# Optimization experiments

Hardware: AMD Instinct MI355X
Metric: run time of the kernel (lower is better)

Reference implementation:

```python
import jax, jax.numpy as jnp
import numpy as np

B, P, T = 128, 196, 20
VOCAB, ENC, EMB, DEC, ATTN = 10000, 2048, 512, 512, 512


def _linear_params(key, out_dim, in_dim):
    kw, kb = jax.random.split(key)
    s = 1.0 / np.sqrt(in_dim)
    W = jax.random.uniform(kw, (out_dim, in_dim), minval=-s, maxval=s, dtype=jnp.float32)
    b = jax.random.uniform(kb, (out_dim,), minval=-s, maxval=s, dtype=jnp.float32)
    return W, b


def setup_inputs() -> dict:
    key = jax.random.key(0)
    ks = jax.random.split(key, 12)
    enc_w, enc_b = _linear_params(ks[0], ATTN, ENC)
    dec_w, dec_b = _linear_params(ks[1], ATTN, DEC)
    full_w, full_b = _linear_params(ks[2], 1, ATTN)
    W_ih, b_ih = _linear_params(ks[3], 4 * DEC, EMB + ENC)
    W_hh, b_hh = _linear_params(ks[4], 4 * DEC, DEC)
    ih_w, ih_b = _linear_params(ks[5], DEC, ENC)
    ic_w, ic_b = _linear_params(ks[6], DEC, ENC)
    fc_w, fc_b = _linear_params(ks[7], VOCAB, DEC)
    return {
        "encoder_out": jax.random.normal(ks[8], (B, P, ENC), dtype=jnp.float32),
        "captions": jax.random.randint(ks[9], (B, T), 0, VOCAB, dtype=jnp.int32),
        "lengths": jax.random.randint(ks[10], (B,), 1, T + 1, dtype=jnp.int32),
        "embedding": jax.random.normal(ks[11], (VOCAB, EMB), dtype=jnp.float32),
        "enc_attn_w": enc_w, "enc_attn_b": enc_b,
        "dec_attn_w": dec_w, "dec_attn_b": dec_b,
        "full_attn_w": full_w, "full_attn_b": full_b,
        "W_ih": W_ih, "b_ih": b_ih, "W_hh": W_hh, "b_hh": b_hh,
        "init_h_w": ih_w, "init_h_b": ih_b,
        "init_c_w": ic_w, "init_c_b": ic_b,
        "fc_w": fc_w, "fc_b": fc_b,
    }


def reference(encoder_out, captions, lengths, embedding,
              enc_attn_w, enc_attn_b, dec_attn_w, dec_attn_b,
              full_attn_w, full_attn_b, W_ih, b_ih, W_hh, b_hh,
              init_h_w, init_h_b, init_c_w, init_c_b, fc_w, fc_b):
    # init hidden state from mean-pooled encoder features
    mean_enc = encoder_out.mean(axis=1)                      # [B, ENC]
    h = mean_enc @ init_h_w.T + init_h_b                      # [B, DEC]
    c = mean_enc @ init_c_w.T + init_c_b

    # loop-invariant encoder projection for additive attention
    attn_enc = jnp.einsum('bpe,ae->bpa', encoder_out, enc_attn_w) + enc_attn_b  # [B, P, ATTN]

    embs = embedding[captions]                                # [B, T, EMB]
    embs_t = jnp.swapaxes(embs, 0, 1)                         # [T, B, EMB]

    dec = h.shape[1]

    def step(carry, emb_t):
        h, c = carry
        # additive attention
        attn_dec = h @ dec_attn_w.T + dec_attn_b              # [B, ATTN]
        energy = jnp.einsum('bpa,a->bp', jax.nn.relu(attn_enc + attn_dec[:, None, :]), full_attn_w[0]) + full_attn_b[0]
        alpha = jax.nn.softmax(energy, axis=1)                # [B, P]
        context = jnp.einsum('bpe,bp->be', encoder_out, alpha)  # [B, ENC]
        # LSTMCell
        x = jnp.concatenate([emb_t, context], axis=1)
        gates = x @ W_ih.T + b_ih + h @ W_hh.T + b_hh          # [B, 4*DEC]
        i, f, g, o = jnp.split(gates, 4, axis=1)
        c_new = jax.nn.sigmoid(f) * c + jax.nn.sigmoid(i) * jnp.tanh(g)
        h_new = jax.nn.sigmoid(o) * jnp.tanh(c_new)
        preds = h_new @ fc_w.T + fc_b                          # [B, VOCAB] (dropout in eval mode = identity)
        return (h_new, c_new), (preds, alpha)

    (_, _), (outputs_t, alphas_t) = jax.lax.scan(step, (h, c), embs_t)
    outputs = jnp.swapaxes(outputs_t, 0, 1)                   # [B, T, VOCAB]
    alphas = jnp.swapaxes(alphas_t, 0, 1)                     # [B, T, P]
    return outputs, alphas
```

## Files before the change

kernel.cpp:

```cpp
#include <hip/hip_runtime.h>

constexpr int kB = 128, kP = 196, kT = 20;
constexpr int kVocab = 10000, kEnc = 2048, kEmb = 512, kDec = 512, kAttn = 512;

typedef __bf16 b16x8 __attribute__((ext_vector_type(8)));
typedef __bf16 b16x4 __attribute__((ext_vector_type(4)));
typedef float f32x4 __attribute__((ext_vector_type(4)));
typedef unsigned short u16x4 __attribute__((ext_vector_type(4)));

__device__ __forceinline__ unsigned short f2bf(float f) {
  unsigned int u = __float_as_uint(f);
  u += 0x7fffu + ((u >> 16) & 1u);
  return (unsigned short)(u >> 16);
}
__device__ __forceinline__ float bf2f(unsigned short h) {
  return __uint_as_float(((unsigned int)h) << 16);
}

__device__ __forceinline__ void async16(const void* g, void* l) {
  __builtin_amdgcn_global_load_lds(
      (const __attribute__((address_space(1))) unsigned int*)g,
      (__attribute__((address_space(3))) unsigned int*)l, 16, 0, 0);
}

__global__ __launch_bounds__(256) void gemm_ae(
    const unsigned short* __restrict__ A, const unsigned short* __restrict__ W,
    const float* __restrict__ bias, unsigned short* __restrict__ Cb, int M, int K) {
  __shared__ unsigned short sA[128 * 32];
  const int tid = threadIdx.x;
  const int lane = tid & 63, wave = tid >> 6;
  const int m0 = blockIdx.y * 128;
  const int n0 = blockIdx.x * 64;
  const int q = lane >> 4, l = lane & 15;
  const int ch0 = tid >> 7, row0 = tid & 127;
  f32x4 acc[2][4] = {};

  for (int k0 = 0; k0 < K; k0 += 32) {
    async16(A + (long)(m0 + row0) * K + k0 + ch0 * 8, &sA[(ch0 * 128 + row0) * 8]);
    async16(A + (long)(m0 + row0) * K + k0 + (ch0 + 2) * 8, &sA[((ch0 + 2) * 128 + row0) * 8]);
    b16x8 bf4[4];
#pragma unroll
    for (int j = 0; j < 4; j++)
      bf4[j] = *(const b16x8*)(W + (long)(n0 + 16 * j + l) * K + k0 + q * 8);
    __syncthreads();
    b16x8 af[2];
#pragma unroll
    for (int i = 0; i < 2; i++)
      af[i] = *(const b16x8*)&sA[(q * 128 + wave * 32 + 16 * i + l) * 8];
#pragma unroll
    for (int i = 0; i < 2; i++)
#pragma unroll
      for (int j = 0; j < 4; j++)
        acc[i][j] = __builtin_amdgcn_mfma_f32_16x16x32_bf16(af[i], bf4[j], acc[i][j], 0, 0, 0);
    __syncthreads();
  }

#pragma unroll
  for (int i = 0; i < 2; i++)
#pragma unroll
    for (int j = 0; j < 4; j++) {
      const int col = n0 + 16 * j + l;
      const float bv = bias[col];
#pragma unroll
      for (int r = 0; r < 4; r++) {
        const int row = m0 + wave * 32 + 16 * i + q * 4 + r;
        Cb[(long)row * 512 + col] = f2bf(acc[i][j][r] + bv);
      }
    }
}

template <bool A_BF16, bool OUT_BF16>
__global__ __launch_bounds__(256) void gemm_bt(
    const void* __restrict__ A_, const unsigned short* __restrict__ W,
    const float* __restrict__ bias, float* __restrict__ C,
    unsigned short* __restrict__ Cb, int M, int N, int K, long ldc) {
  const int lane = threadIdx.x & 63;
  const int wave = threadIdx.x >> 6;
  const int wm = wave >> 1, wn = wave & 1;
  const int m0 = blockIdx.y * 64 + wm * 32;
  const int n0 = blockIdx.x * 64 + wn * 32;
  const int q = lane >> 4;
  const int l = lane & 15;
  f32x4 acc[2][2] = {};
  const unsigned short* Ab = (const unsigned short*)A_;
  const float* Af = (const float*)A_;

  for (int k0 = 0; k0 < K; k0 += 32) {
    const int ka = k0 + q * 8;
    b16x8 af[2], wf[2];
#pragma unroll
    for (int i = 0; i < 2; i++) {
      int r = m0 + 16 * i + l;
      if (r >= M) r = M - 1;
      if (A_BF16) {
        af[i] = *(const b16x8*)(Ab + (long)r * K + ka);
      } else {
        const float* p = Af + (long)r * K + ka;
        const f32x4 lo = *(const f32x4*)p;
        const f32x4 hi = *(const f32x4*)(p + 4);
        b16x8 t;
#pragma unroll
        for (int j = 0; j < 4; j++) {
          ((unsigned short*)&t)[j] = f2bf(lo[j]);
          ((unsigned short*)&t)[4 + j] = f2bf(hi[j]);
        }
        af[i] = t;
      }
    }
#pragma unroll
    for (int j = 0; j < 2; j++) {
      int r = n0 + 16 * j + l;
      if (r >= N) r = N - 1;
      wf[j] = *(const b16x8*)(W + (long)r * K + ka);
    }
#pragma unroll
    for (int i = 0; i < 2; i++)
#pragma unroll
      for (int j = 0; j < 2; j++)
        acc[i][j] = __builtin_amdgcn_mfma_f32_16x16x32_bf16(af[i], wf[j], acc[i][j], 0, 0, 0);
  }

#pragma unroll
  for (int i = 0; i < 2; i++)
#pragma unroll
    for (int j = 0; j < 2; j++) {
      const int col = n0 + 16 * j + l;
      if (col >= N) continue;
      const float bv = bias ? bias[col] : 0.0f;
#pragma unroll
      for (int r = 0; r < 4; r++) {
        const int row = m0 + 16 * i + q * 4 + r;
        if (row >= M) continue;
        const float v = acc[i][j][r] + bv;
        if (OUT_BF16) Cb[(long)row * ldc + col] = f2bf(v);
        else          C[(long)row * ldc + col] = v;
      }
    }
}

__global__ __launch_bounds__(256) void adfc_kernel(
    const unsigned short* __restrict__ h_bf,
    const unsigned short* __restrict__ daw, const float* __restrict__ dab,
    float* __restrict__ ad_out,
    const unsigned short* __restrict__ fcw, const float* __restrict__ fcb,
    float* __restrict__ preds, long pred_ld) {
  const int blk = blockIdx.x;
  const unsigned short* W;
  const float* bias;
  float* out;
  long ldc;
  int N, m0, n0;
  if (blk < 16) {
    if (!ad_out) return;
    W = daw; bias = dab; out = ad_out; ldc = 512; N = 512;
    n0 = (blk & 7) * 64; m0 = (blk >> 3) * 64;
  } else {
    if (!preds) return;
    const int idx = blk - 16;
    W = fcw; bias = fcb; out = preds; ldc = pred_ld; N = kVocab;
    n0 = (idx % 157) * 64; m0 = (idx / 157) * 64;
  }
  const int lane = threadIdx.x & 63, wave = threadIdx.x >> 6;
  const int wm = wave >> 1, wn = wave & 1;
  const int q = lane >> 4, l = lane & 15;
  const int mi = m0 + wm * 32, ni = n0 + wn * 32;
  f32x4 acc[2][2] = {};

  for (int k0 = 0; k0 < 512; k0 += 64) {
    b16x8 af[2][2], wf[2][2];
#pragma unroll
    for (int u = 0; u < 2; u++) {
      const int ka = k0 + u * 32 + q * 8;
#pragma unroll
      for (int i = 0; i < 2; i++)
        af[u][i] = *(const b16x8*)(h_bf + (long)(mi + 16 * i + l) * 512 + ka);
#pragma unroll
      for (int j = 0; j < 2; j++) {
        int r = ni + 16 * j + l;
        if (r >= N) r = N - 1;
        wf[u][j] = *(const b16x8*)(W + (long)r * 512 + ka);
      }
    }
#pragma unroll
    for (int u = 0; u < 2; u++)
#pragma unroll
      for (int i = 0; i < 2; i++)
#pragma unroll
        for (int j = 0; j < 2; j++)
          acc[i][j] = __builtin_amdgcn_mfma_f32_16x16x32_bf16(af[u][i], wf[u][j], acc[i][j], 0, 0, 0);
  }
#pragma unroll
  for (int i = 0; i < 2; i++)
#pragma unroll
    for (int j = 0; j < 2; j++) {
      const int col = ni + 16 * j + l;
      if (col >= N) continue;
      const float bv = bias[col];
#pragma unroll
      for (int r = 0; r < 4; r++) {
        const int row = mi + 16 * i + q * 4 + r;
        out[(long)row * ldc + col] = acc[i][j][r] + bv;
      }
    }
}

template <bool SRC_BF16>
__global__ __launch_bounds__(256) void attn2(
    const void* __restrict__ enc_, const unsigned short* __restrict__ attn_enc_bf,
    const float* __restrict__ ad_g, const float* __restrict__ faw,
    const float* __restrict__ fab, float* __restrict__ alphas,
    unsigned short* __restrict__ ctx, int t) {
  const int b = blockIdx.x;
  const int half = blockIdx.y;
  const int tid = threadIdx.x;
  const int lane = tid & 63, wave = tid >> 6;
  __shared__ float ad_s[512];
  __shared__ float e_sm[kP];
  __shared__ float red[4];
  __shared__ float cred[128][8];

  ad_s[tid] = ad_g[b * kAttn + tid];
  ad_s[tid + 256] = ad_g[b * kAttn + tid + 256];
  __syncthreads();

  float ad8[8], w8[8];
  const int a0 = lane * 8;
#pragma unroll
  for (int j = 0; j < 8; j++) { ad8[j] = ad_s[a0 + j]; w8[j] = faw[a0 + j]; }
  const float fb0 = fab[0];
  for (int p = wave; p < kP; p += 4) {
    const b16x8 rv = *(const b16x8*)(attn_enc_bf + ((long)(b * kP + p)) * kAttn + a0);
    float s = 0.f;
#pragma unroll
    for (int j = 0; j < 8; j++)
      s += w8[j] * fmaxf(bf2f(((const unsigned short*)&rv)[j]) + ad8[j], 0.f);
#pragma unroll
    for (int off = 32; off > 0; off >>= 1) s += __shfl_down(s, off, 64);
    if (lane == 0) e_sm[p] = s + fb0;
  }
  __syncthreads();

  const float v = (tid < kP) ? e_sm[tid] : -3.0e38f;
  float m = v;
#pragma unroll
  for (int off = 32; off > 0; off >>= 1) m = fmaxf(m, __shfl_down(m, off, 64));
  if (lane == 0) red[wave] = m;
  __syncthreads();
  m = fmaxf(fmaxf(red[0], red[1]), fmaxf(red[2], red[3]));
  const float ex = (tid < kP) ? expf(v - m) : 0.f;
  float s = ex;
#pragma unroll
  for (int off = 32; off > 0; off >>= 1) s += __shfl_down(s, off, 64);
  if (lane == 0) red[wave] = s;
  __syncthreads();
  s = red[0] + red[1] + red[2] + red[3];
  __syncthreads();
  const float alpha = ex / s;
  if (tid < kP) {
    e_sm[tid] = alpha;
    if (half == 0) alphas[((long)b * kT + t) * kP + tid] = alpha;
  }
  __syncthreads();

  const int pg = tid >> 7, th = tid & 127;
  const int e = half * 1024 + th * 8;
  float a8[8] = {};
  if (SRC_BF16) {
    const unsigned short* base = (const unsigned short*)enc_ + (long)b * kP * kEnc + e;
    const int pbeg = pg * 98;
#pragma unroll 2
    for (int p = pbeg; p < pbeg + 98; p++) {
      const float a = e_sm[p];
      const b16x8 rv = *(const b16x8*)(base + (long)p * kEnc);
#pragma unroll
      for (int j = 0; j < 8; j++) a8[j] += a * bf2f(((const unsigned short*)&rv)[j]);
    }
  } else {
    const float* base = (const float*)enc_ + (long)b * kP * kEnc + e;
    const int pbeg = pg * 98;
#pragma unroll 2
    for (int p = pbeg; p < pbeg + 98; p++) {
      const float a = e_sm[p];
      const f32x4 lo = *(const f32x4*)(base + (long)p * kEnc);
      const f32x4 hi = *(const f32x4*)(base + (long)p * kEnc + 4);
#pragma unroll
      for (int j = 0; j < 4; j++) { a8[j] += a * lo[j]; a8[4 + j] += a * hi[j]; }
    }
  }
  if (pg == 1) {
#pragma unroll
    for (int j = 0; j < 8; j++) cred[th][j] = a8[j];
  }
  __syncthreads();
  if (pg == 0) {
    u16x4 o0, o1;
#pragma unroll
    for (int j = 0; j < 4; j++) {
      o0[j] = f2bf(a8[j] + cred[th][j]);
      o1[j] = f2bf(a8[4 + j] + cred[th][4 + j]);
    }
    *(u16x4*)(ctx + (long)b * kEnc + e) = o0;
    *(u16x4*)(ctx + (long)b * kEnc + e + 4) = o1;
  }
}

__global__ __launch_bounds__(256) void gemm_gates(
    const unsigned short* __restrict__ embs_t, const unsigned short* __restrict__ ctx,
    const unsigned short* __restrict__ hbf, const unsigned short* __restrict__ Wih,
    const unsigned short* __restrict__ Whh, float* __restrict__ gates_part) {
  const int lane = threadIdx.x & 63;
  const int wave = threadIdx.x >> 6;
  const int wm = wave >> 1, wn = wave & 1;
  const int m0 = blockIdx.y * 64 + wm * 32;
  const int n0 = blockIdx.x * 64 + wn * 32;
  const int z = blockIdx.z;
  const int q = lane >> 4;
  const int l = lane & 15;
  f32x4 acc[2][2] = {};
  float* gout = gates_part + (long)z * kB * 2048;

  const int kbeg = z * 768, kend = kbeg + 768;
  for (int k0 = kbeg; k0 < kend; k0 += 32) {
    b16x8 af[2], wf[2];
#pragma unroll
    for (int i = 0; i < 2; i++) {
      const int r = m0 + 16 * i + l;
      const unsigned short* p;
      if (k0 < 512)        p = embs_t + (long)r * kEmb + k0;
      else if (k0 < 2560)  p = ctx + (long)r * kEnc + (k0 - 512);
      else                 p = hbf + (long)r * kDec + (k0 - 2560);
      af[i] = *(const b16x8*)(p + q * 8);
    }
#pragma unroll
    for (int j = 0; j < 2; j++) {
      const int r = n0 + 16 * j + l;
      const unsigned short* p;
      if (k0 < 2560) p = Wih + (long)r * 2560 + k0;
      else           p = Whh + (long)r * 512 + (k0 - 2560);
      wf[j] = *(const b16x8*)(p + q * 8);
    }
#pragma unroll
    for (int i = 0; i < 2; i++)
#pragma unroll
      for (int j = 0; j < 2; j++)
        acc[i][j] = __builtin_amdgcn_mfma_f32_16x16x32_bf16(af[i], wf[j], acc[i][j], 0, 0, 0);
  }
#pragma unroll
  for (int i = 0; i < 2; i++)
#pragma unroll
    for (int j = 0; j < 2; j++) {
      const int col = n0 + 16 * j + l;
#pragma unroll
      for (int r = 0; r < 4; r++) {
        const int row = m0 + 16 * i + q * 4 + r;
        gout[(long)row * 2048 + col] = acc[i][j][r];
      }
    }
}

__global__ __launch_bounds__(256) void lstm_pw(
    const float* __restrict__ gp, const float* __restrict__ bsum,
    float* __restrict__ c, float* __restrict__ h, unsigned short* __restrict__ hbf) {
  const int idx = blockIdx.x * 256 + threadIdx.x;
  const int b = idx >> 9, d = idx & 511;
  float g4[4];
#pragma unroll
  for (int g = 0; g < 4; g++) {
    const int col = g * 512 + d;
    float s = bsum[col];
#pragma unroll
    for (int z = 0; z < 4; z++) s += gp[(long)z * kB * 2048 + (long)b * 2048 + col];
    g4[g] = s;
  }
  const float si = 1.f / (1.f + expf(-g4[0]));
  const float sf = 1.f / (1.f + expf(-g4[1]));
  const float so = 1.f / (1.f + expf(-g4[3]));
  const float cn = sf * c[idx] + si * tanhf(g4[2]);
  const float hn = so * tanhf(cn);
  c[idx] = cn;
  h[idx] = hn;
  hbf[idx] = f2bf(hn);
}

template <bool SRC_BF16>
__global__ __launch_bounds__(256) void mean_kernel(
    const void* __restrict__ enc_, unsigned short* __restrict__ mean_bf) {
  const int b = blockIdx.x;
  const int e = threadIdx.x * 8;
  float acc[8] = {};
  if (SRC_BF16) {
    const unsigned short* base = (const unsigned short*)enc_ + (long)b * kP * kEnc + e;
    for (int p = 0; p < kP; p++) {
      const b16x8 v = *(const b16x8*)(base + (long)p * kEnc);
#pragma unroll
      for (int j = 0; j < 8; j++) acc[j] += bf2f(((const unsigned short*)&v)[j]);
    }
  } else {
    const float* base = (const float*)enc_ + (long)b * kP * kEnc + e;
    for (int p = 0; p < kP; p++) {
      const f32x4 lo = *(const f32x4*)(base + (long)p * kEnc);
      const f32x4 hi = *(const f32x4*)(base + (long)p * kEnc + 4);
#pragma unroll
      for (int j = 0; j < 4; j++) { acc[j] += lo[j]; acc[4 + j] += hi[j]; }
    }
  }
#pragma unroll
  for (int j = 0; j < 8; j++)
    mean_bf[(long)b * kEnc + e + j] = f2bf(acc[j] * (1.0f / 196.0f));
}

__global__ __launch_bounds__(256) void f32_to_bf16_vec(
    const float* __restrict__ src, unsigned short* __restrict__ dst, long n4) {
  for (long i = blockIdx.x * (long)blockDim.x + threadIdx.x; i < n4;
       i += (long)gridDim.x * blockDim.x) {
    const f32x4 v = *(const f32x4*)(src + i * 4);
    u16x4 o;
#pragma unroll
    for (int j = 0; j < 4; j++) o[j] = f2bf(v[j]);
    *(u16x4*)(dst + i * 4) = o;
  }
}

__global__ __launch_bounds__(256) void gather_emb(
    const float* __restrict__ embedding, const int* __restrict__ captions,
    unsigned short* __restrict__ embs) {
  const int r = blockIdx.x;
  const int t = r >> 7, b = r & 127;
  const int cap = captions[b * kT + t];
  const float* src = embedding + (long)cap * kEmb;
  unsigned short* dst = embs + (long)r * kEmb;
  for (int i = threadIdx.x; i < kEmb; i += 256) dst[i] = f2bf(src[i]);
}

__global__ void bias_sum_k(const float* __restrict__ b1, const float* __restrict__ b2,
                           float* __restrict__ o) {
  const int i = blockIdx.x * 256 + threadIdx.x;
  if (i < 2048) o[i] = b1[i] + b2[i];
}

extern "C" void kernel_launch(void* const* d_in, const int* in_sizes, int n_in,
                              void* d_out, int out_size, void* d_ws, size_t ws_size,
                              hipStream_t stream) {
  const float* enc = (const float*)d_in[0];
  const int* captions = (const int*)d_in[1];
  const float* embedding = (const float*)d_in[3];
  const float* eaw = (const float*)d_in[4];
  const float* eab = (const float*)d_in[5];
  const float* daw = (const float*)d_in[6];
  const float* dab = (const float*)d_in[7];
  const float* faw = (const float*)d_in[8];
  const float* fab = (const float*)d_in[9];
  const float* Wih = (const float*)d_in[10];
  const float* bih = (const float*)d_in[11];
  const float* Whh = (const float*)d_in[12];
  const float* bhh = (const float*)d_in[13];
  const float* ihw = (const float*)d_in[14];
  const float* ihb = (const float*)d_in[15];
  const float* icw = (const float*)d_in[16];
  const float* icb = (const float*)d_in[17];
  const float* fcw = (const float*)d_in[18];
  const float* fcb = (const float*)d_in[19];

  float* out = (float*)d_out;
  float* alphas = out + (long)kB * kT * kVocab;

  char* ws = (char*)d_ws;
  size_t off = 0;
  auto alloc = [&](size_t bytes) -> void* {
    void* p = ws + off;
    off = (off + bytes + 255) & ~(size_t)255;
    return p;
  };
  unsigned short* attn_enc_bf = (unsigned short*)alloc((size_t)kB * kP * kAttn * 2);
  unsigned short* Wih_bf = (unsigned short*)alloc((size_t)2048 * 2560 * 2);
  unsigned short* Whh_bf = (unsigned short*)alloc((size_t)2048 * 512 * 2);
  unsigned short* fcw_bf = (unsigned short*)alloc((size_t)kVocab * kDec * 2);
  unsigned short* eaw_bf = (unsigned short*)alloc((size_t)kAttn * kEnc * 2);
  unsigned short* daw_bf = (unsigned short*)alloc((size_t)kAttn * kDec * 2);
  unsigned short* ihw_bf = (unsigned short*)alloc((size_t)kDec * kEnc * 2);
  unsigned short* icw_bf = (unsigned short*)alloc((size_t)kDec * kEnc * 2);
  unsigned short* embs_bf = (unsigned short*)alloc((size_t)kT * kB * kEmb * 2);
  unsigned short* mean_bf = (unsigned short*)alloc((size_t)kB * kEnc * 2);
  float* h = (float*)alloc((size_t)kB * kDec * 4);
  float* c = (float*)alloc((size_t)kB * kDec * 4);
  unsigned short* h_bf = (unsigned short*)alloc((size_t)kB * kDec * 2);
  float* ad_buf = (float*)alloc((size_t)kB * kAttn * 4);
  unsigned short* ctx_bf = (unsigned short*)alloc((size_t)kB * kEnc * 2);
  float* gates_part = (float*)alloc((size_t)4 * kB * 2048 * 4);
  float* bsum = (float*)alloc((size_t)2048 * 4);
  unsigned short* enc_bf = (unsigned short*)alloc((size_t)kB * kP * kEnc * 2);
  const bool have_enc_bf = (off <= ws_size);

  auto cvt = [&](const float* s, unsigned short* d, long n) {
    const long n4 = n / 4;
    long g = (n4 + 255) / 256;
    if (g > 2048) g = 2048;
    f32_to_bf16_vec<<<dim3((unsigned)g), dim3(256), 0, stream>>>(s, d, n4);
  };

  cvt(eaw, eaw_bf, (long)kAttn * kEnc);
  cvt(daw, daw_bf, (long)kAttn * kDec);
  cvt(Wih, Wih_bf, (long)2048 * 2560);
  cvt(Whh, Whh_bf, (long)2048 * 512);
  cvt(fcw, fcw_bf, (long)kVocab * kDec);
  cvt(ihw, ihw_bf, (long)kDec * kEnc);
  cvt(icw, icw_bf, (long)kDec * kEnc);
  if (have_enc_bf) cvt(enc, enc_bf, (long)kB * kP * kEnc);
  bias_sum_k<<<8, 256, 0, stream>>>(bih, bhh, bsum);
  gather_emb<<<kT * kB, 256, 0, stream>>>(embedding, captions, embs_bf);
  if (have_enc_bf)
    mean_kernel<true><<<kB, 256, 0, stream>>>(enc_bf, mean_bf);
  else
    mean_kernel<false><<<kB, 256, 0, stream>>>(enc, mean_bf);

  gemm_bt<true, false><<<dim3(kDec / 64, kB / 64), 256, 0, stream>>>(
      mean_bf, ihw_bf, ihb, h, (unsigned short*)nullptr, kB, kDec, kEnc, kDec);
  gemm_bt<true, false><<<dim3(kDec / 64, kB / 64), 256, 0, stream>>>(
      mean_bf, icw_bf, icb, c, (unsigned short*)nullptr, kB, kDec, kEnc, kDec);
  cvt(h, h_bf, (long)kB * kDec);

  if (have_enc_bf)
    gemm_ae<<<dim3(kAttn / 64, (kB * kP) / 128), 256, 0, stream>>>(
        enc_bf, eaw_bf, eab, attn_enc_bf, kB * kP, kEnc);
  else
    gemm_bt<false, true><<<dim3(kAttn / 64, (kB * kP) / 64), 256, 0, stream>>>(
        enc, eaw_bf, eab, (float*)nullptr, attn_enc_bf, kB * kP, kAttn, kEnc, kAttn);

  for (int t = 0; t < kT; t++) {
    adfc_kernel<<<330, 256, 0, stream>>>(
        h_bf, daw_bf, dab, ad_buf, fcw_bf, fcb,
        (t == 0) ? (float*)nullptr : out + (long)(t - 1) * kVocab, (long)kT * kVocab);

    if (have_enc_bf)
      attn2<true><<<dim3(kB, 2), 256, 0, stream>>>(
          enc_bf, attn_enc_bf, ad_buf, faw, fab, alphas, ctx_bf, t);
    else
      attn2<false><<<dim3(kB, 2), 256, 0, stream>>>(
          enc, attn_enc_bf, ad_buf, faw, fab, alphas, ctx_bf, t);

    gemm_gates<<<dim3(2048 / 64, kB / 64, 4), 256, 0, stream>>>(
        embs_bf + (long)t * kB * kEmb, ctx_bf, h_bf, Wih_bf, Whh_bf, gates_part);

    lstm_pw<<<(kB * kDec) / 256, 256, 0, stream>>>(gates_part, bsum, c, h, h_bf);
  }
  adfc_kernel<<<330, 256, 0, stream>>>(
      h_bf, daw_bf, dab, (float*)nullptr, fcw_bf, fcb,
      out + (long)19 * kVocab, (long)kT * kVocab);
}
```

Measured before the change: 2.444 ms.

## Hoist vocab projection out of recurrence into one batched GEMM; retile encoder projection

Each step's bf16 hidden state is now kept in a history buffer. The per-step output-vocabulary projection is removed from the scan loop and replaced by one 128x128-tiled MFMA GEMM over all timesteps after the loop. That GEMM scatters rows into the [B, T, VOCAB] output layout. The per-step adfc launch shrinks to only the decoder-attention part, which shortens the serial critical path. The encoder attention projection also moves to the same 128x128 kernel, which stages W through LDS for more reuse. One risk: the last vocab tile reads weight rows past row 10000 into adjacent workspace memory, although those columns are masked on store.

```diff
diff --git a/kernel.cpp b/kernel.cpp
--- a/kernel.cpp
+++ b/kernel.cpp
@@ -23,50 +23,68 @@
       (__attribute__((address_space(3))) unsigned int*)l, 16, 0, 0);
 }
 
-__global__ __launch_bounds__(256) void gemm_ae(
+template <int MODE>
+__global__ __launch_bounds__(256) void gemm128(
     const unsigned short* __restrict__ A, const unsigned short* __restrict__ W,
-    const float* __restrict__ bias, unsigned short* __restrict__ Cb, int M, int K) {
+    const float* __restrict__ bias, unsigned short* __restrict__ Cb,
+    float* __restrict__ Cf, int K, int Nv) {
   __shared__ unsigned short sA[128 * 32];
+  __shared__ unsigned short sB[128 * 32];
   const int tid = threadIdx.x;
   const int lane = tid & 63, wave = tid >> 6;
-  const int m0 = blockIdx.y * 128;
-  const int n0 = blockIdx.x * 64;
+  const int wm = wave >> 1, wn = wave & 1;
   const int q = lane >> 4, l = lane & 15;
-  const int ch0 = tid >> 7, row0 = tid & 127;
-  f32x4 acc[2][4] = {};
+  const int m0 = blockIdx.y * 128, n0 = blockIdx.x * 128;
+  const int row0 = tid & 127, ch0 = tid >> 7;
+  const long arow = (long)(m0 + row0) * K + ch0 * 8;
+  const long brow = (long)(n0 + row0) * K + ch0 * 8;
+  unsigned short* sAd0 = &sA[(ch0 * 128 + row0) * 8];
+  unsigned short* sAd1 = &sA[((ch0 + 2) * 128 + row0) * 8];
+  unsigned short* sBd0 = &sB[(ch0 * 128 + row0) * 8];
+  unsigned short* sBd1 = &sB[((ch0 + 2) * 128 + row0) * 8];
+  f32x4 acc[4][4] = {};
 
   for (int k0 = 0; k0 < K; k0 += 32) {
-    async16(A + (long)(m0 + row0) * K + k0 + ch0 * 8, &sA[(ch0 * 128 + row0) * 8]);
-    async16(A + (long)(m0 + row0) * K + k0 + (ch0 + 2) * 8, &sA[((ch0 + 2) * 128 + row0) * 8]);
-    b16x8 bf4[4];
+    async16(A + arow + k0, sAd0);
+    async16(A + arow + k0 + 16, sAd1);
+    async16(W + brow + k0, sBd0);
+    async16(W + brow + k0 + 16, sBd1);
+    __syncthreads();
+    b16x8 af[4], bf[4];
+#pragma unroll
+    for (int i = 0; i < 4; i++)
+      af[i] = *(const b16x8*)&sA[(q * 128 + wm * 64 + 16 * i + l) * 8];
 #pragma unroll
     for (int j = 0; j < 4; j++)
-      bf4[j] = *(const b16x8*)(W + (long)(n0 + 16 * j + l) * K + k0 + q * 8);
+      bf[j] = *(const b16x8*)&sB[(q * 128 + wn * 64 + 16 * j + l) * 8];
+#pragma unroll
+    for (int i = 0; i < 4; i++)
+#pragma unroll
+      for (int j = 0; j < 4; j++)
+        acc[i][j] = __builtin_amdgcn_mfma_f32_16x16x32_bf16(af[i], bf[j], acc[i][j], 0, 0, 0);
     __syncthreads();
-    b16x8 af[2];
-#pragma unroll
-    for (int i = 0; i < 2; i++)
-      af[i] = *(const b16x8*)&sA[(q * 128 + wave * 32 + 16 * i + l) * 8];
-#pragma unroll
-    for (int i = 0; i < 2; i++)
-#pragma unroll
-      for (int j = 0; j < 4; j++)
-        acc[i][j] = __builtin_amdgcn_mfma_f32_16x16x32_bf16(af[i], bf4[j], acc[i][j], 0, 0, 0);
-    __syncthreads();
-  }
-
-#pragma unroll
-  for (int i = 0; i < 2; i++)
+  }
+
+#pragma unroll
+  for (int i = 0; i < 4; i++) {
+    const int row = m0 + wm * 64 + 16 * i + q * 4;
 #pragma unroll
     for (int j = 0; j < 4; j++) {
-      const int col = n0 + 16 * j + l;
+      const int col = n0 + wn * 64 + 16 * j + l;
+      if (col >= Nv) continue;
       const float bv = bias[col];
 #pragma unroll
       for (int r = 0; r < 4; r++) {
-        const int row = m0 + wave * 32 + 16 * i + q * 4 + r;
-        Cb[(long)row * 512 + col] = f2bf(acc[i][j][r] + bv);
+        const float v = acc[i][j][r] + bv;
+        if (MODE == 0) {
+          Cb[(long)(row + r) * kAttn + col] = f2bf(v);
+        } else {
+          const int rr = row + r;
+          Cf[((long)(rr & 127) * kT + (rr >> 7)) * (long)kVocab + col] = v;
+        }
       }
     }
+  }
 }
 
 template <bool A_BF16, bool OUT_BF16>
@@ -483,7 +501,7 @@
   unsigned short* mean_bf = (unsigned short*)alloc((size_t)kB * kEnc * 2);
   float* h = (float*)alloc((size_t)kB * kDec * 4);
   float* c = (float*)alloc((size_t)kB * kDec * 4);
-  unsigned short* h_bf = (unsigned short*)alloc((size_t)kB * kDec * 2);
+  unsigned short* h_hist = (unsigned short*)alloc((size_t)(kT + 1) * kB * kDec * 2);
   float* ad_buf = (float*)alloc((size_t)kB * kAttn * 4);
   unsigned short* ctx_bf = (unsigned short*)alloc((size_t)kB * kEnc * 2);
   float* gates_part = (float*)alloc((size_t)4 * kB * 2048 * 4);
@@ -517,19 +535,20 @@
       mean_bf, ihw_bf, ihb, h, (unsigned short*)nullptr, kB, kDec, kEnc, kDec);
   gemm_bt<true, false><<<dim3(kDec / 64, kB / 64), 256, 0, stream>>>(
       mean_bf, icw_bf, icb, c, (unsigned short*)nullptr, kB, kDec, kEnc, kDec);
-  cvt(h, h_bf, (long)kB * kDec);
+  cvt(h, h_hist, (long)kB * kDec);
 
   if (have_enc_bf)
-    gemm_ae<<<dim3(kAttn / 64, (kB * kP) / 128), 256, 0, stream>>>(
-        enc_bf, eaw_bf, eab, attn_enc_bf, kB * kP, kEnc);
+    gemm128<0><<<dim3(kAttn / 128, (kB * kP) / 128), 256, 0, stream>>>(
+        enc_bf, eaw_bf, eab, attn_enc_bf, (float*)nullptr, kEnc, kAttn);
   else
     gemm_bt<false, true><<<dim3(kAttn / 64, (kB * kP) / 64), 256, 0, stream>>>(
         enc, eaw_bf, eab, (float*)nullptr, attn_enc_bf, kB * kP, kAttn, kEnc, kAttn);
 
   for (int t = 0; t < kT; t++) {
-    adfc_kernel<<<330, 256, 0, stream>>>(
-        h_bf, daw_bf, dab, ad_buf, fcw_bf, fcb,
-        (t == 0) ? (float*)nullptr : out + (long)(t - 1) * kVocab, (long)kT * kVocab);
+    const unsigned short* hcur = h_hist + (long)t * kB * kDec;
+
+    adfc_kernel<<<16, 256, 0, stream>>>(
+        hcur, daw_bf, dab, ad_buf, fcw_bf, fcb, (float*)nullptr, 0);
 
     if (have_enc_bf)
       attn2<true><<<dim3(kB, 2), 256, 0, stream>>>(
@@ -539,11 +558,12 @@
           enc, attn_enc_bf, ad_buf, faw, fab, alphas, ctx_bf, t);
 
     gemm_gates<<<dim3(2048 / 64, kB / 64, 4), 256, 0, stream>>>(
-        embs_bf + (long)t * kB * kEmb, ctx_bf, h_bf, Wih_bf, Whh_bf, gates_part);
-
-    lstm_pw<<<(kB * kDec) / 256, 256, 0, stream>>>(gates_part, bsum, c, h, h_bf);
-  }
-  adfc_kernel<<<330, 256, 0, stream>>>(
-      h_bf, daw_bf, dab, (float*)nullptr, fcw_bf, fcb,
-      out + (long)19 * kVocab, (long)kT * kVocab);
-}
+        embs_bf + (long)t * kB * kEmb, ctx_bf, hcur, Wih_bf, Whh_bf, gates_part);
+
+    lstm_pw<<<(kB * kDec) / 256, 256, 0, stream>>>(
+        gates_part, bsum, c, h, h_hist + (long)(t + 1) * kB * kDec);
+  }
+
+  gemm128<1><<<dim3((kVocab + 127) / 128, kT * kB / 128), 256, 0, stream>>>(
+      h_hist + (long)kB * kDec, fcw_bf, fcb, (unsigned short*)nullptr, out, kDec, kVocab);
+}
```

Result: faster. 2.200 ms (-10.0%).
